# Performance work log

Measured on AMD Instinct MI355X. Metric: run time of the kernel, lower is better.

## Reference

```python
import jax, jax.numpy as jnp
import numpy as np

EPS = 1e-12  # F.normalize eps


def _normalize(x, axis):
    n = jnp.linalg.norm(x, axis=axis, keepdims=True)
    return x / jnp.maximum(n, EPS)


def _channel_equi_vec_normalize(x):
    # x: [B, C, 3, N]
    x_dir = _normalize(x, axis=2)
    x_norm = jnp.linalg.norm(x, axis=2, keepdims=True)   # [B,C,1,N]
    x_nn = _normalize(x_norm, axis=1)
    return x_dir * x_nn


def _se3_w(W):
    # append last column so each row sums to 1
    return jnp.concatenate([W, 1.0 - W.sum(-1, keepdims=True)], axis=-1)


def _vlin(W, x):
    # W: [O, C], x: [B, C, 3, N] -> [B, O, 3, N]
    return jnp.einsum('oc,bcvn->bovn', W, x)


def _slin(W, b, s):
    # W: [O, C], s: [B, C, N] -> [B, O, N]
    return jnp.einsum('oc,bcn->bon', W, s) + b[None, :, None]


def setup_inputs() -> dict:
    key = jax.random.key(0)
    ks = jax.random.split(key, 12)
    B, C, N = 16, 128, 4096
    scale = 0.05
    return {
        'v_input': jax.random.normal(ks[0], (B, C, 3, N), jnp.float32),
        's_input': jax.random.normal(ks[1], (B, C, N), jnp.float32),
        'weight': jax.random.normal(ks[2], (C, C - 1), jnp.float32) * scale,
        'sv_W': jax.random.normal(ks[3], (C, C), jnp.float32) * scale,
        'sv_b': jax.random.normal(ks[4], (C,), jnp.float32) * scale,
        'cross_weight': jax.random.normal(ks[5], (C, C - 1), jnp.float32) * scale,
        'crossfc_weight': jax.random.normal(ks[6], (C, 2 * C - 1), jnp.float32) * scale,
        'vsdir_weight': jax.random.normal(ks[7], (C, C), jnp.float32) * scale,
        'vs_W': jax.random.normal(ks[8], (C, C), jnp.float32) * scale,
        'vs_b': jax.random.normal(ks[9], (C,), jnp.float32) * scale,
        'ss_W': jax.random.normal(ks[10], (C, C), jnp.float32) * scale,
        'ss_b': jax.random.normal(ks[11], (C,), jnp.float32) * scale,
    }


def reference(v_input, s_input, weight, sv_W, sv_b, cross_weight, crossfc_weight,
              vsdir_weight, vs_W, vs_b, ss_W, ss_b):
    # --- vector output (se3 linear over channels) ---
    v_out = _vlin(_se3_w(weight), v_input)                       # [B,O,3,N]

    # --- scalar -> vector invariant scaling (se3: center, scale, re-add mean) ---
    s2v = _normalize(jnp.einsum('os,bsn->bon', sv_W, s_input) + sv_b[None, :, None], axis=1)
    v_mean = v_out.mean(axis=1, keepdims=True)
    v_out = (v_out - v_mean) * s2v[:, :, None, :] + v_mean

    # --- cross branch (se3) ---
    v_dual = _vlin(_se3_w(cross_weight), v_input)
    d_o = v_dual.mean(axis=1, keepdims=True)
    v_o = v_out.mean(axis=1, keepdims=True)
    v_cross = jnp.cross(_channel_equi_vec_normalize(v_dual - d_o), v_out - v_o, axis=2)
    v_cross = v_cross + v_out
    v_out = _vlin(_se3_w(crossfc_weight), jnp.concatenate([v_cross, v_out], axis=1))

    # --- scalar output ---
    v_sR = v_input - v_input.mean(axis=1, keepdims=True)         # se3 centering
    dual_dir = _normalize(jnp.einsum('oc,bcvn->bovn', vsdir_weight, v_sR), axis=2)
    s_from_v = _normalize((v_sR * dual_dir).sum(axis=2), axis=1)  # [B,C,N]
    s_from_v = _slin(vs_W, vs_b, s_from_v)
    s_from_s = _slin(ss_W, ss_b, s_input)
    s_output = s_from_s + s_from_v

    return (v_out, s_output)
```

## Files before the change

### kernel.cpp

```cpp
#include <hip/hip_runtime.h>
#include <math.h>

typedef __attribute__((ext_vector_type(8))) short short8;
typedef __attribute__((ext_vector_type(4))) float floatx4;

#define EPS 1e-12f

#define WS_AMAIN 0
#define WS_ASCAL 51200
#define WS_AFC   83968
#define WS_AVS   116736
#define WS_VDR_B 266240

__device__ __forceinline__ unsigned short f2bf(float f) {
  union { float f; unsigned u; } v; v.f = f;
  unsigned r = v.u + 0x7FFFu + ((v.u >> 16) & 1u);
  return (unsigned short)(r >> 16);
}
__device__ __forceinline__ float bf2f(unsigned u16) {
  union { unsigned u; float f; } v; v.u = u16 << 16;
  return v.f;
}

__device__ __forceinline__ float block_sum_256(float v, float* red) {
  const int t = threadIdx.x;
  red[t] = v;
  __syncthreads();
  for (int s = 128; s > 0; s >>= 1) {
    if (t < s) red[t] += red[t + s];
    __syncthreads();
  }
  float r = red[0];
  __syncthreads();
  return r;
}

__global__ __launch_bounds__(256) void k_pre(
    const float* __restrict__ weight, const float* __restrict__ sv_W,
    const float* __restrict__ cross_w, const float* __restrict__ crossfc_w,
    const float* __restrict__ vsdir_w, const float* __restrict__ vs_W,
    const float* __restrict__ ss_W, unsigned short* __restrict__ wsu,
    float* __restrict__ vdr) {
  __shared__ float red[256];
  const int o = blockIdx.x;
  const int t = threadIdx.x;

  float s1 = block_sum_256((t < 127) ? weight[o * 127 + t] : 0.f, red);
  if (t < 128)
    wsu[WS_AMAIN + o * 128 + t] = f2bf((t < 127) ? weight[o * 127 + t] : 1.f - s1);

  float s2 = block_sum_256((t < 127) ? cross_w[o * 127 + t] : 0.f, red);
  if (t < 128)
    wsu[WS_AMAIN + (128 + o) * 128 + t] = f2bf((t < 127) ? cross_w[o * 127 + t] : 1.f - s2);

  float s4 = block_sum_256((t < 128) ? vsdir_w[o * 128 + t] : 0.f, red);
  if (t < 128)
    wsu[WS_AMAIN + (256 + o) * 128 + t] = f2bf(vsdir_w[o * 128 + t]);
  if (t == 0) vdr[o] = s4;

  float s3 = block_sum_256((t < 255) ? crossfc_w[o * 255 + t] : 0.f, red);
  wsu[WS_AFC + o * 256 + t] = f2bf((t < 255) ? crossfc_w[o * 255 + t] : 1.f - s3);

  if (t < 128) {
    wsu[WS_ASCAL + o * 128 + t]         = f2bf(sv_W[o * 128 + t]);
    wsu[WS_ASCAL + (128 + o) * 128 + t] = f2bf(ss_W[o * 128 + t]);
    wsu[WS_AVS + o * 128 + t]           = f2bf(vs_W[o * 128 + t]);
  }
  if (o == 0) {
    if (t < 128) wsu[WS_AMAIN + 386 * 128 + t] = f2bf(1.f / 128.f);
    for (int l = t; l < 13 * 128; l += 256) wsu[WS_AMAIN + 387 * 128 + l] = 0;
  }
}

__global__ void k_mean(unsigned short* __restrict__ wsu) {
  const int g = blockIdx.x, c = threadIdx.x;
  float s = 0.f;
  for (int o = 0; o < 128; ++o) s += bf2f(wsu[WS_AMAIN + (g * 128 + o) * 128 + c]);
  wsu[WS_AMAIN + (384 + g) * 128 + c] = f2bf(s * (1.f / 128.f));
}

__global__ __launch_bounds__(512, 2) void k_main(
    const float* __restrict__ v_in, const float* __restrict__ s_in,
    const unsigned short* __restrict__ wsu, const float* __restrict__ vdr,
    const float* __restrict__ sv_b, const float* __restrict__ vs_b,
    const float* __restrict__ ss_b,
    float* __restrict__ v_out, float* __restrict__ s_out) {
  const int t = threadIdx.x;
  const int wave = t >> 6, lane = t & 63;
  const int q = lane >> 4, ln = lane & 15;
  const int cg = wave & 3;
  const int rg = wave >> 2;
  const int b = blockIdx.x >> 6;
  const int n0 = (blockIdx.x & 63) * 64;
  const int mycol = cg * 16 + ln;
  const int rb = rg * 64;
  const int rc = cg * 16 + ln;

  __shared__ __align__(16) unsigned short xB[192 * 136];
  __shared__ __align__(16) unsigned short v2B[192 * 136];
  __shared__ __align__(16) unsigned short sB[64 * 136];
  __shared__ float xred[6][2][64];

  {
    const float* vb = v_in + (size_t)b * (128 * 3 * 4096) + n0;
    for (int l = t; l < 6144; l += 512) {
      const int c = l / 48, r = l % 48;
      const int v = r >> 4, j4 = (r & 15) * 4;
      const float4 f = *(const float4*)(vb + (size_t)(c * 3 + v) * 4096 + j4);
      const int base = (v * 64 + j4) * 136 + c;
      xB[base]       = f2bf(f.x);
      xB[base + 136] = f2bf(f.y);
      xB[base + 272] = f2bf(f.z);
      xB[base + 408] = f2bf(f.w);
    }
    const float* sb = s_in + (size_t)b * (128 * 4096) + n0;
    for (int l = t; l < 2048; l += 512) {
      const int c = l >> 4, j4 = (l & 15) * 4;
      const float4 f = *(const float4*)(sb + (size_t)c * 4096 + j4);
      const int base = j4 * 136 + c;
      sB[base]       = f2bf(f.x);
      sB[base + 136] = f2bf(f.y);
      sB[base + 272] = f2bf(f.z);
      sB[base + 408] = f2bf(f.w);
    }
  }
  __syncthreads();

  floatx4 accS[8];
#pragma unroll
  for (int i = 0; i < 8; ++i) accS[i] = (floatx4){0.f, 0.f, 0.f, 0.f};
#pragma unroll
  for (int k = 0; k < 4; ++k) {
    const short8 bf = *(const short8*)(sB + mycol * 136 + k * 32 + q * 8);
    const unsigned short* ap = wsu + WS_ASCAL + (rb + ln) * 128 + k * 32 + q * 8;
#pragma unroll
    for (int mt = 0; mt < 4; ++mt)
      accS[mt] = __builtin_amdgcn_mfma_f32_16x16x32_bf16(
          *(const short8*)(ap + mt * 2048), bf, accS[mt], 0, 0, 0);
    const unsigned short* ap2 = ap + 128 * 128;
#pragma unroll
    for (int mt = 0; mt < 4; ++mt)
      accS[4 + mt] = __builtin_amdgcn_mfma_f32_16x16x32_bf16(
          *(const short8*)(ap2 + mt * 2048), bf, accS[4 + mt], 0, 0, 0);
  }
  float s2v[4][4], tssb[4][4];
  {
    float nrm = 0.f;
#pragma unroll
    for (int mt = 0; mt < 4; ++mt) {
      const float4 bb = *(const float4*)(sv_b + rb + mt * 16 + q * 4);
      const float* bp = (const float*)&bb;
#pragma unroll
      for (int r = 0; r < 4; ++r) {
        const float tv = accS[mt][r] + bp[r];
        s2v[mt][r] = tv;
        nrm += tv * tv;
      }
    }
    nrm += __shfl_xor(nrm, 16);
    nrm += __shfl_xor(nrm, 32);
    if (lane < 16) xred[0][rg][rc] = nrm;
    __syncthreads();
    const float ntot = xred[0][0][rc] + xred[0][1][rc];
    const float inv = 1.f / fmaxf(sqrtf(ntot), EPS);
#pragma unroll
    for (int mt = 0; mt < 4; ++mt)
#pragma unroll
      for (int r = 0; r < 4; ++r) s2v[mt][r] *= inv;
#pragma unroll
    for (int mt = 0; mt < 4; ++mt) {
      const float4 b1 = *(const float4*)(ss_b + rb + mt * 16 + q * 4);
      const float4 b2 = *(const float4*)(vs_b + rb + mt * 16 + q * 4);
      const float* p1 = (const float*)&b1;
      const float* p2 = (const float*)&b2;
#pragma unroll
      for (int r = 0; r < 4; ++r) tssb[mt][r] = accS[4 + mt][r] + p1[r] + p2[r];
    }
  }

  floatx4 accD[5][3];
#pragma unroll
  for (int i = 0; i < 5; ++i)
#pragma unroll
    for (int v = 0; v < 3; ++v) accD[i][v] = (floatx4){0.f, 0.f, 0.f, 0.f};
#pragma unroll
  for (int k = 0; k < 4; ++k) {
    short8 bfv[3];
#pragma unroll
    for (int v = 0; v < 3; ++v)
      bfv[v] = *(const short8*)(xB + (v * 64 + mycol) * 136 + k * 32 + q * 8);
    const unsigned short* ap = wsu + WS_AMAIN + (256 + rb + ln) * 128 + k * 32 + q * 8;
#pragma unroll
    for (int i = 0; i < 4; ++i) {
      const short8 a = *(const short8*)(ap + i * 2048);
#pragma unroll
      for (int v = 0; v < 3; ++v)
        accD[i][v] = __builtin_amdgcn_mfma_f32_16x16x32_bf16(a, bfv[v], accD[i][v], 0, 0, 0);
    }
    const unsigned short* am = wsu + WS_AMAIN + (384 + ln) * 128 + k * 32 + q * 8;
    const short8 a4 = *(const short8*)am;
#pragma unroll
    for (int v = 0; v < 3; ++v)
      accD[4][v] = __builtin_amdgcn_mfma_f32_16x16x32_bf16(a4, bfv[v], accD[4][v], 0, 0, 0);
  }
  float xm[3], vmn[3], dmn[3];
#pragma unroll
  for (int v = 0; v < 3; ++v) {
    vmn[v] = __shfl(accD[4][v][0], ln);
    dmn[v] = __shfl(accD[4][v][1], ln);
    xm[v]  = __shfl(accD[4][v][2], ln);
  }

  {
    float sfv[4][4];
    float ssum = 0.f;
#pragma unroll
    for (int mt = 0; mt < 4; ++mt) {
      const float4 rs4 = *(const float4*)(vdr + rb + mt * 16 + q * 4);
      const float* rp = (const float*)&rs4;
      uint2 pk[3];
#pragma unroll
      for (int v = 0; v < 3; ++v)
        pk[v] = *(const uint2*)(xB + (v * 64 + mycol) * 136 + rb + mt * 16 + q * 4);
#pragma unroll
      for (int r = 0; r < 4; ++r) {
        float d[3], xr[3];
#pragma unroll
        for (int v = 0; v < 3; ++v) {
          d[v] = accD[mt][v][r] - rp[r] * xm[v];
          const unsigned w = (r < 2) ? pk[v].x : pk[v].y;
          xr[v] = bf2f((w >> ((r & 1) * 16)) & 0xffffu) - xm[v];
        }
        const float n2 = d[0] * d[0] + d[1] * d[1] + d[2] * d[2];
        const float dinv = 1.f / fmaxf(sqrtf(n2), EPS);
        const float sv_ = (xr[0] * d[0] + xr[1] * d[1] + xr[2] * d[2]) * dinv;
        sfv[mt][r] = sv_;
        ssum += sv_ * sv_;
      }
    }
    ssum += __shfl_xor(ssum, 16);
    ssum += __shfl_xor(ssum, 32);
    if (lane < 16) xred[1][rg][rc] = ssum;
    __syncthreads();
    const float stot = xred[1][0][rc] + xred[1][1][rc];
    const float sinv = 1.f / fmaxf(sqrtf(stot), EPS);
#pragma unroll
    for (int mt = 0; mt < 4; ++mt) {
      const unsigned lo = (unsigned)f2bf(sfv[mt][0] * sinv) |
                          ((unsigned)f2bf(sfv[mt][1] * sinv) << 16);
      const unsigned hi = (unsigned)f2bf(sfv[mt][2] * sinv) |
                          ((unsigned)f2bf(sfv[mt][3] * sinv) << 16);
      *(uint2*)(sB + mycol * 136 + rb + mt * 16 + q * 4) = make_uint2(lo, hi);
    }
  }

  floatx4 accV[4][3];
#pragma unroll
  for (int i = 0; i < 4; ++i)
#pragma unroll
    for (int v = 0; v < 3; ++v) accV[i][v] = (floatx4){0.f, 0.f, 0.f, 0.f};
#pragma unroll
  for (int k = 0; k < 4; ++k) {
    short8 bfv[3];
#pragma unroll
    for (int v = 0; v < 3; ++v)
      bfv[v] = *(const short8*)(xB + (v * 64 + mycol) * 136 + k * 32 + q * 8);
    const unsigned short* ap = wsu + WS_AMAIN + (rb + ln) * 128 + k * 32 + q * 8;
#pragma unroll
    for (int mt = 0; mt < 4; ++mt) {
      const short8 a = *(const short8*)(ap + mt * 2048);
#pragma unroll
      for (int v = 0; v < 3; ++v)
        accV[mt][v] = __builtin_amdgcn_mfma_f32_16x16x32_bf16(a, bfv[v], accV[mt][v], 0, 0, 0);
    }
  }
  float v2m[3];
#pragma unroll
  for (int v = 0; v < 3; ++v) {
    float s = 0.f;
#pragma unroll
    for (int mt = 0; mt < 4; ++mt)
#pragma unroll
      for (int r = 0; r < 4; ++r) {
        const float val = (accV[mt][v][r] - vmn[v]) * s2v[mt][r] + vmn[v];
        accV[mt][v][r] = val;
        s += val;
      }
    s += __shfl_xor(s, 16);
    s += __shfl_xor(s, 32);
    if (lane < 16) xred[2 + v][rg][rc] = s;
  }
  __syncthreads();
#pragma unroll
  for (int v = 0; v < 3; ++v)
    v2m[v] = (xred[2 + v][0][rc] + xred[2 + v][1][rc]) * (1.f / 128.f);
#pragma unroll
  for (int mt = 0; mt < 4; ++mt)
#pragma unroll
    for (int v = 0; v < 3; ++v) {
      const unsigned lo = (unsigned)f2bf(accV[mt][v][0]) |
                          ((unsigned)f2bf(accV[mt][v][1]) << 16);
      const unsigned hi = (unsigned)f2bf(accV[mt][v][2]) |
                          ((unsigned)f2bf(accV[mt][v][3]) << 16);
      *(uint2*)(v2B + (v * 64 + mycol) * 136 + rb + mt * 16 + q * 4) = make_uint2(lo, hi);
    }

  floatx4 accW[4][3];
#pragma unroll
  for (int i = 0; i < 4; ++i)
#pragma unroll
    for (int v = 0; v < 3; ++v) accW[i][v] = (floatx4){0.f, 0.f, 0.f, 0.f};
#pragma unroll
  for (int k = 0; k < 4; ++k) {
    short8 bfv[3];
#pragma unroll
    for (int v = 0; v < 3; ++v)
      bfv[v] = *(const short8*)(xB + (v * 64 + mycol) * 136 + k * 32 + q * 8);
    const unsigned short* ap = wsu + WS_AMAIN + (128 + rb + ln) * 128 + k * 32 + q * 8;
#pragma unroll
    for (int mt = 0; mt < 4; ++mt) {
      const short8 a = *(const short8*)(ap + mt * 2048);
#pragma unroll
      for (int v = 0; v < 3; ++v)
        accW[mt][v] = __builtin_amdgcn_mfma_f32_16x16x32_bf16(a, bfv[v], accW[mt][v], 0, 0, 0);
    }
  }
  float an[4][4];
  float csum = 0.f;
#pragma unroll
  for (int mt = 0; mt < 4; ++mt)
#pragma unroll
    for (int r = 0; r < 4; ++r) {
      const float a0 = accW[mt][0][r] - dmn[0];
      const float a1 = accW[mt][1][r] - dmn[1];
      const float a2 = accW[mt][2][r] - dmn[2];
      accW[mt][0][r] = a0; accW[mt][1][r] = a1; accW[mt][2][r] = a2;
      const float n2 = a0 * a0 + a1 * a1 + a2 * a2;
      an[mt][r] = sqrtf(n2);
      csum += n2;
    }
  csum += __shfl_xor(csum, 16);
  csum += __shfl_xor(csum, 32);
  if (lane < 16) xred[5][rg][rc] = csum;
  __syncthreads();
  const float ctot = xred[5][0][rc] + xred[5][1][rc];
  const float cninv = 1.f / fmaxf(sqrtf(ctot), EPS);
#pragma unroll
  for (int mt = 0; mt < 4; ++mt) {
    float crv[3][4];
#pragma unroll
    for (int r = 0; r < 4; ++r) {
      const float sc = an[mt][r] / fmaxf(an[mt][r], EPS) * cninv;
      const float h0 = accW[mt][0][r] * sc;
      const float h1 = accW[mt][1][r] * sc;
      const float h2 = accW[mt][2][r] * sc;
      const float w0 = accV[mt][0][r], w1 = accV[mt][1][r], w2 = accV[mt][2][r];
      const float g0 = w0 - v2m[0], g1 = w1 - v2m[1], g2 = w2 - v2m[2];
      crv[0][r] = h1 * g2 - h2 * g1 + w0;
      crv[1][r] = h2 * g0 - h0 * g2 + w1;
      crv[2][r] = h0 * g1 - h1 * g0 + w2;
    }
#pragma unroll
    for (int v = 0; v < 3; ++v) {
      const unsigned lo = (unsigned)f2bf(crv[v][0]) | ((unsigned)f2bf(crv[v][1]) << 16);
      const unsigned hi = (unsigned)f2bf(crv[v][2]) | ((unsigned)f2bf(crv[v][3]) << 16);
      *(uint2*)(xB + (v * 64 + mycol) * 136 + rb + mt * 16 + q * 4) = make_uint2(lo, hi);
    }
  }
  __syncthreads();

  floatx4 accO[4][3];
  floatx4 accP[4];
#pragma unroll
  for (int i = 0; i < 4; ++i) {
    accP[i] = (floatx4){0.f, 0.f, 0.f, 0.f};
#pragma unroll
    for (int v = 0; v < 3; ++v) accO[i][v] = (floatx4){0.f, 0.f, 0.f, 0.f};
  }
#pragma unroll
  for (int ks = 0; ks < 8; ++ks) {
    const unsigned short* src = (ks < 4) ? xB : v2B;
    const int kk = ks & 3;
    short8 bfv[3];
#pragma unroll
    for (int v = 0; v < 3; ++v)
      bfv[v] = *(const short8*)(src + (v * 64 + mycol) * 136 + kk * 32 + q * 8);
    const unsigned short* afc = wsu + WS_AFC + (rb + ln) * 256 + ks * 32 + q * 8;
#pragma unroll
    for (int mt = 0; mt < 4; ++mt) {
      const short8 a = *(const short8*)(afc + mt * 4096);
#pragma unroll
      for (int v = 0; v < 3; ++v)
        accO[mt][v] = __builtin_amdgcn_mfma_f32_16x16x32_bf16(a, bfv[v], accO[mt][v], 0, 0, 0);
    }
    if (ks < 4) {
      const short8 bfs = *(const short8*)(sB + mycol * 136 + kk * 32 + q * 8);
      const unsigned short* avs = wsu + WS_AVS + (rb + ln) * 128 + kk * 32 + q * 8;
#pragma unroll
      for (int mt = 0; mt < 4; ++mt)
        accP[mt] = __builtin_amdgcn_mfma_f32_16x16x32_bf16(
            *(const short8*)(avs + mt * 2048), bfs, accP[mt], 0, 0, 0);
    }
  }

  const int gc = n0 + mycol;
  float* vob = v_out + (size_t)b * (128 * 3 * 4096) + gc;
  float* sob = s_out + (size_t)b * (128 * 4096) + gc;
#pragma unroll
  for (int mt = 0; mt < 4; ++mt)
#pragma unroll
    for (int r = 0; r < 4; ++r) {
      const int o = rb + mt * 16 + q * 4 + r;
#pragma unroll
      for (int v = 0; v < 3; ++v)
        vob[(size_t)(o * 3 + v) * 4096] = accO[mt][v][r];
      sob[(size_t)o * 4096] = accP[mt][r] + tssb[mt][r];
    }
}

extern "C" void kernel_launch(void* const* d_in, const int* in_sizes, int n_in,
                              void* d_out, int out_size, void* d_ws, size_t ws_size,
                              hipStream_t stream) {
  const float* v_in      = (const float*)d_in[0];
  const float* s_in      = (const float*)d_in[1];
  const float* weight    = (const float*)d_in[2];
  const float* sv_W      = (const float*)d_in[3];
  const float* sv_b      = (const float*)d_in[4];
  const float* cross_w   = (const float*)d_in[5];
  const float* crossfc_w = (const float*)d_in[6];
  const float* vsdir_w   = (const float*)d_in[7];
  const float* vs_W      = (const float*)d_in[8];
  const float* vs_b      = (const float*)d_in[9];
  const float* ss_W      = (const float*)d_in[10];
  const float* ss_b      = (const float*)d_in[11];

  float* out = (float*)d_out;
  float* v_out = out;
  float* s_out = out + (size_t)16 * 128 * 3 * 4096;
  unsigned short* wsu = (unsigned short*)d_ws;
  float* vdr = (float*)((char*)d_ws + WS_VDR_B);

  hipLaunchKernelGGL(k_pre, dim3(128), dim3(256), 0, stream,
                     weight, sv_W, cross_w, crossfc_w, vsdir_w, vs_W, ss_W, wsu, vdr);
  hipLaunchKernelGGL(k_mean, dim3(2), dim3(128), 0, stream, wsu);
  hipLaunchKernelGGL(k_main, dim3(1024), dim3(512), 0, stream,
                     v_in, s_in, wsu, vdr, sv_b, vs_b, ss_b, v_out, s_out);
}
```

Baseline: 410.1 us.

## Shrink k_main tile to 16 columns, compute channel means in-kernel, drop k_mean

Each block of k_main now handles 16 points instead of 64, and each of the 8 waves owns 16 output rows. This cuts register and shared-memory use so that up to 8 blocks can run per CU, and the grid grows to 4096 blocks with a swizzled block-to-tile mapping. The separate k_mean kernel is removed: the v_out and v_dual channel means are now computed algebraically from in-block reductions over 8 wave groups, and the mean rows of the weight matrix are zeroed. Packed bf16 conversion via v_cvt_pk_bf16_f32 replaces the scalar rounding. The trade-off is more cross-wave reductions and syncs, and the weight rows are reread per block across many more blocks.

```diff
diff --git a/kernel.cpp b/kernel.cpp
--- a/kernel.cpp
+++ b/kernel.cpp
@@ -20,6 +20,11 @@
 __device__ __forceinline__ float bf2f(unsigned u16) {
   union { unsigned u; float f; } v; v.u = u16 << 16;
   return v.f;
+}
+__device__ __forceinline__ unsigned pk2bf(float lo, float hi) {
+  unsigned r;
+  asm("v_cvt_pk_bf16_f32 %0, %1, %2" : "=v"(r) : "v"(lo), "v"(hi));
+  return r;
 }
 
 __device__ __forceinline__ float block_sum_256(float v, float* red) {
@@ -67,19 +72,12 @@
     wsu[WS_AVS + o * 128 + t]           = f2bf(vs_W[o * 128 + t]);
   }
   if (o == 0) {
+    for (int l = t; l < 16 * 128; l += 256) wsu[WS_AMAIN + 384 * 128 + l] = 0;
     if (t < 128) wsu[WS_AMAIN + 386 * 128 + t] = f2bf(1.f / 128.f);
-    for (int l = t; l < 13 * 128; l += 256) wsu[WS_AMAIN + 387 * 128 + l] = 0;
-  }
-}
-
-__global__ void k_mean(unsigned short* __restrict__ wsu) {
-  const int g = blockIdx.x, c = threadIdx.x;
-  float s = 0.f;
-  for (int o = 0; o < 128; ++o) s += bf2f(wsu[WS_AMAIN + (g * 128 + o) * 128 + c]);
-  wsu[WS_AMAIN + (384 + g) * 128 + c] = f2bf(s * (1.f / 128.f));
-}
-
-__global__ __launch_bounds__(512, 2) void k_main(
+  }
+}
+
+__global__ __launch_bounds__(512, 8) void k_main(
     const float* __restrict__ v_in, const float* __restrict__ s_in,
     const unsigned short* __restrict__ wsu, const float* __restrict__ vdr,
     const float* __restrict__ sv_b, const float* __restrict__ vs_b,
@@ -88,99 +86,90 @@
   const int t = threadIdx.x;
   const int wave = t >> 6, lane = t & 63;
   const int q = lane >> 4, ln = lane & 15;
-  const int cg = wave & 3;
-  const int rg = wave >> 2;
-  const int b = blockIdx.x >> 6;
-  const int n0 = (blockIdx.x & 63) * 64;
-  const int mycol = cg * 16 + ln;
-  const int rb = rg * 64;
-  const int rc = cg * 16 + ln;
-
-  __shared__ __align__(16) unsigned short xB[192 * 136];
-  __shared__ __align__(16) unsigned short v2B[192 * 136];
-  __shared__ __align__(16) unsigned short sB[64 * 136];
-  __shared__ float xred[6][2][64];
+  const int rg = wave;
+  const int rb = rg * 16;
+  const int bid = (int)(blockIdx.x & 7) * 512 + (int)(blockIdx.x >> 3);
+  const int b = bid >> 8;
+  const int n0 = (bid & 255) * 16;
+
+  __shared__ __align__(16) unsigned short xB[48 * 136];
+  __shared__ __align__(16) unsigned short v2B[48 * 136];
+  __shared__ __align__(16) unsigned short sB[16 * 136];
+  __shared__ float xred[12][8][16];
 
   {
     const float* vb = v_in + (size_t)b * (128 * 3 * 4096) + n0;
-    for (int l = t; l < 6144; l += 512) {
-      const int c = l / 48, r = l % 48;
-      const int v = r >> 4, j4 = (r & 15) * 4;
+    for (int l = t; l < 1536; l += 512) {
+      const int c = l / 12, rr = l % 12;
+      const int v = rr >> 2, j4 = (rr & 3) * 4;
       const float4 f = *(const float4*)(vb + (size_t)(c * 3 + v) * 4096 + j4);
-      const int base = (v * 64 + j4) * 136 + c;
-      xB[base]       = f2bf(f.x);
-      xB[base + 136] = f2bf(f.y);
-      xB[base + 272] = f2bf(f.z);
-      xB[base + 408] = f2bf(f.w);
+      const int base = (v * 16 + j4) * 136 + c;
+      const unsigned p01 = pk2bf(f.x, f.y);
+      const unsigned p23 = pk2bf(f.z, f.w);
+      xB[base]       = (unsigned short)p01;
+      xB[base + 136] = (unsigned short)(p01 >> 16);
+      xB[base + 272] = (unsigned short)p23;
+      xB[base + 408] = (unsigned short)(p23 >> 16);
     }
     const float* sb = s_in + (size_t)b * (128 * 4096) + n0;
-    for (int l = t; l < 2048; l += 512) {
-      const int c = l >> 4, j4 = (l & 15) * 4;
+    {
+      const int c = t >> 2, j4 = (t & 3) * 4;
       const float4 f = *(const float4*)(sb + (size_t)c * 4096 + j4);
       const int base = j4 * 136 + c;
-      sB[base]       = f2bf(f.x);
-      sB[base + 136] = f2bf(f.y);
-      sB[base + 272] = f2bf(f.z);
-      sB[base + 408] = f2bf(f.w);
-    }
-  }
-  __syncthreads();
-
-  floatx4 accS[8];
-#pragma unroll
-  for (int i = 0; i < 8; ++i) accS[i] = (floatx4){0.f, 0.f, 0.f, 0.f};
+      const unsigned p01 = pk2bf(f.x, f.y);
+      const unsigned p23 = pk2bf(f.z, f.w);
+      sB[base]       = (unsigned short)p01;
+      sB[base + 136] = (unsigned short)(p01 >> 16);
+      sB[base + 272] = (unsigned short)p23;
+      sB[base + 408] = (unsigned short)(p23 >> 16);
+    }
+  }
+  __syncthreads();
+
+  floatx4 accS[2];
+  accS[0] = (floatx4){0.f, 0.f, 0.f, 0.f};
+  accS[1] = (floatx4){0.f, 0.f, 0.f, 0.f};
 #pragma unroll
   for (int k = 0; k < 4; ++k) {
-    const short8 bf = *(const short8*)(sB + mycol * 136 + k * 32 + q * 8);
+    const short8 bf = *(const short8*)(sB + ln * 136 + k * 32 + q * 8);
     const unsigned short* ap = wsu + WS_ASCAL + (rb + ln) * 128 + k * 32 + q * 8;
-#pragma unroll
-    for (int mt = 0; mt < 4; ++mt)
-      accS[mt] = __builtin_amdgcn_mfma_f32_16x16x32_bf16(
-          *(const short8*)(ap + mt * 2048), bf, accS[mt], 0, 0, 0);
-    const unsigned short* ap2 = ap + 128 * 128;
-#pragma unroll
-    for (int mt = 0; mt < 4; ++mt)
-      accS[4 + mt] = __builtin_amdgcn_mfma_f32_16x16x32_bf16(
-          *(const short8*)(ap2 + mt * 2048), bf, accS[4 + mt], 0, 0, 0);
-  }
-  float s2v[4][4], tssb[4][4];
+    accS[0] = __builtin_amdgcn_mfma_f32_16x16x32_bf16(
+        *(const short8*)ap, bf, accS[0], 0, 0, 0);
+    accS[1] = __builtin_amdgcn_mfma_f32_16x16x32_bf16(
+        *(const short8*)(ap + 128 * 128), bf, accS[1], 0, 0, 0);
+  }
+  float s2v[4], tssb[4];
   {
     float nrm = 0.f;
-#pragma unroll
-    for (int mt = 0; mt < 4; ++mt) {
-      const float4 bb = *(const float4*)(sv_b + rb + mt * 16 + q * 4);
-      const float* bp = (const float*)&bb;
-#pragma unroll
-      for (int r = 0; r < 4; ++r) {
-        const float tv = accS[mt][r] + bp[r];
-        s2v[mt][r] = tv;
-        nrm += tv * tv;
-      }
+    const float4 bb = *(const float4*)(sv_b + rb + q * 4);
+    const float* bp = (const float*)&bb;
+#pragma unroll
+    for (int r = 0; r < 4; ++r) {
+      const float tv = accS[0][r] + bp[r];
+      s2v[r] = tv;
+      nrm += tv * tv;
     }
     nrm += __shfl_xor(nrm, 16);
     nrm += __shfl_xor(nrm, 32);
-    if (lane < 16) xred[0][rg][rc] = nrm;
+    if (lane < 16) xred[0][rg][ln] = nrm;
     __syncthreads();
-    const float ntot = xred[0][0][rc] + xred[0][1][rc];
+    float ntot = 0.f;
+#pragma unroll
+    for (int g = 0; g < 8; ++g) ntot += xred[0][g][ln];
     const float inv = 1.f / fmaxf(sqrtf(ntot), EPS);
 #pragma unroll
-    for (int mt = 0; mt < 4; ++mt)
-#pragma unroll
-      for (int r = 0; r < 4; ++r) s2v[mt][r] *= inv;
-#pragma unroll
-    for (int mt = 0; mt < 4; ++mt) {
-      const float4 b1 = *(const float4*)(ss_b + rb + mt * 16 + q * 4);
-      const float4 b2 = *(const float4*)(vs_b + rb + mt * 16 + q * 4);
-      const float* p1 = (const float*)&b1;
-      const float* p2 = (const float*)&b2;
-#pragma unroll
-      for (int r = 0; r < 4; ++r) tssb[mt][r] = accS[4 + mt][r] + p1[r] + p2[r];
-    }
-  }
-
-  floatx4 accD[5][3];
-#pragma unroll
-  for (int i = 0; i < 5; ++i)
+    for (int r = 0; r < 4; ++r) s2v[r] *= inv;
+    const float4 b1 = *(const float4*)(ss_b + rb + q * 4);
+    const float4 b2 = *(const float4*)(vs_b + rb + q * 4);
+    const float* p1 = (const float*)&b1;
+    const float* p2 = (const float*)&b2;
+#pragma unroll
+    for (int r = 0; r < 4; ++r) tssb[r] = accS[1][r] + p1[r] + p2[r];
+  }
+
+  floatx4 accD[2][3];
+#pragma unroll
+  for (int i = 0; i < 2; ++i)
 #pragma unroll
     for (int v = 0; v < 3; ++v) accD[i][v] = (floatx4){0.f, 0.f, 0.f, 0.f};
 #pragma unroll
@@ -188,173 +177,176 @@
     short8 bfv[3];
 #pragma unroll
     for (int v = 0; v < 3; ++v)
-      bfv[v] = *(const short8*)(xB + (v * 64 + mycol) * 136 + k * 32 + q * 8);
+      bfv[v] = *(const short8*)(xB + (v * 16 + ln) * 136 + k * 32 + q * 8);
     const unsigned short* ap = wsu + WS_AMAIN + (256 + rb + ln) * 128 + k * 32 + q * 8;
-#pragma unroll
-    for (int i = 0; i < 4; ++i) {
-      const short8 a = *(const short8*)(ap + i * 2048);
-#pragma unroll
-      for (int v = 0; v < 3; ++v)
-        accD[i][v] = __builtin_amdgcn_mfma_f32_16x16x32_bf16(a, bfv[v], accD[i][v], 0, 0, 0);
-    }
+    const short8 a0 = *(const short8*)ap;
     const unsigned short* am = wsu + WS_AMAIN + (384 + ln) * 128 + k * 32 + q * 8;
-    const short8 a4 = *(const short8*)am;
-#pragma unroll
-    for (int v = 0; v < 3; ++v)
-      accD[4][v] = __builtin_amdgcn_mfma_f32_16x16x32_bf16(a4, bfv[v], accD[4][v], 0, 0, 0);
-  }
-  float xm[3], vmn[3], dmn[3];
-#pragma unroll
-  for (int v = 0; v < 3; ++v) {
-    vmn[v] = __shfl(accD[4][v][0], ln);
-    dmn[v] = __shfl(accD[4][v][1], ln);
-    xm[v]  = __shfl(accD[4][v][2], ln);
-  }
-
-  {
-    float sfv[4][4];
+    const short8 a1 = *(const short8*)am;
+#pragma unroll
+    for (int v = 0; v < 3; ++v) {
+      accD[0][v] = __builtin_amdgcn_mfma_f32_16x16x32_bf16(a0, bfv[v], accD[0][v], 0, 0, 0);
+      accD[1][v] = __builtin_amdgcn_mfma_f32_16x16x32_bf16(a1, bfv[v], accD[1][v], 0, 0, 0);
+    }
+  }
+  float xm[3];
+#pragma unroll
+  for (int v = 0; v < 3; ++v) xm[v] = __shfl(accD[1][v][2], ln);
+
+  {
+    float sfv[4];
     float ssum = 0.f;
-#pragma unroll
-    for (int mt = 0; mt < 4; ++mt) {
-      const float4 rs4 = *(const float4*)(vdr + rb + mt * 16 + q * 4);
-      const float* rp = (const float*)&rs4;
-      uint2 pk[3];
-#pragma unroll
-      for (int v = 0; v < 3; ++v)
-        pk[v] = *(const uint2*)(xB + (v * 64 + mycol) * 136 + rb + mt * 16 + q * 4);
-#pragma unroll
-      for (int r = 0; r < 4; ++r) {
-        float d[3], xr[3];
-#pragma unroll
-        for (int v = 0; v < 3; ++v) {
-          d[v] = accD[mt][v][r] - rp[r] * xm[v];
-          const unsigned w = (r < 2) ? pk[v].x : pk[v].y;
-          xr[v] = bf2f((w >> ((r & 1) * 16)) & 0xffffu) - xm[v];
-        }
-        const float n2 = d[0] * d[0] + d[1] * d[1] + d[2] * d[2];
-        const float dinv = 1.f / fmaxf(sqrtf(n2), EPS);
-        const float sv_ = (xr[0] * d[0] + xr[1] * d[1] + xr[2] * d[2]) * dinv;
-        sfv[mt][r] = sv_;
-        ssum += sv_ * sv_;
+    const float4 rs4 = *(const float4*)(vdr + rb + q * 4);
+    const float* rp = (const float*)&rs4;
+    uint2 pk[3];
+#pragma unroll
+    for (int v = 0; v < 3; ++v)
+      pk[v] = *(const uint2*)(xB + (v * 16 + ln) * 136 + rb + q * 4);
+#pragma unroll
+    for (int r = 0; r < 4; ++r) {
+      float d[3], xr[3];
+#pragma unroll
+      for (int v = 0; v < 3; ++v) {
+        d[v] = accD[0][v][r] - rp[r] * xm[v];
+        const unsigned w = (r < 2) ? pk[v].x : pk[v].y;
+        xr[v] = bf2f((w >> ((r & 1) * 16)) & 0xffffu) - xm[v];
       }
+      const float n2 = d[0] * d[0] + d[1] * d[1] + d[2] * d[2];
+      const float dinv = 1.f / fmaxf(sqrtf(n2), EPS);
+      const float sv_ = (xr[0] * d[0] + xr[1] * d[1] + xr[2] * d[2]) * dinv;
+      sfv[r] = sv_;
+      ssum += sv_ * sv_;
     }
     ssum += __shfl_xor(ssum, 16);
     ssum += __shfl_xor(ssum, 32);
-    if (lane < 16) xred[1][rg][rc] = ssum;
+    if (lane < 16) xred[1][rg][ln] = ssum;
     __syncthreads();
-    const float stot = xred[1][0][rc] + xred[1][1][rc];
+    float stot = 0.f;
+#pragma unroll
+    for (int g = 0; g < 8; ++g) stot += xred[1][g][ln];
     const float sinv = 1.f / fmaxf(sqrtf(stot), EPS);
-#pragma unroll
-    for (int mt = 0; mt < 4; ++mt) {
-      const unsigned lo = (unsigned)f2bf(sfv[mt][0] * sinv) |
-                          ((unsigned)f2bf(sfv[mt][1] * sinv) << 16);
-      const unsigned hi = (unsigned)f2bf(sfv[mt][2] * sinv) |
-                          ((unsigned)f2bf(sfv[mt][3] * sinv) << 16);
-      *(uint2*)(sB + mycol * 136 + rb + mt * 16 + q * 4) = make_uint2(lo, hi);
-    }
-  }
-
-  floatx4 accV[4][3];
-#pragma unroll
-  for (int i = 0; i < 4; ++i)
-#pragma unroll
-    for (int v = 0; v < 3; ++v) accV[i][v] = (floatx4){0.f, 0.f, 0.f, 0.f};
+    const unsigned lo = pk2bf(sfv[0] * sinv, sfv[1] * sinv);
+    const unsigned hi = pk2bf(sfv[2] * sinv, sfv[3] * sinv);
+    *(uint2*)(sB + ln * 136 + rb + q * 4) = make_uint2(lo, hi);
+  }
+
+  floatx4 accV[3];
+#pragma unroll
+  for (int v = 0; v < 3; ++v) accV[v] = (floatx4){0.f, 0.f, 0.f, 0.f};
 #pragma unroll
   for (int k = 0; k < 4; ++k) {
     short8 bfv[3];
 #pragma unroll
     for (int v = 0; v < 3; ++v)
-      bfv[v] = *(const short8*)(xB + (v * 64 + mycol) * 136 + k * 32 + q * 8);
+      bfv[v] = *(const short8*)(xB + (v * 16 + ln) * 136 + k * 32 + q * 8);
     const unsigned short* ap = wsu + WS_AMAIN + (rb + ln) * 128 + k * 32 + q * 8;
-#pragma unroll
-    for (int mt = 0; mt < 4; ++mt) {
-      const short8 a = *(const short8*)(ap + mt * 2048);
-#pragma unroll
-      for (int v = 0; v < 3; ++v)
-        accV[mt][v] = __builtin_amdgcn_mfma_f32_16x16x32_bf16(a, bfv[v], accV[mt][v], 0, 0, 0);
-    }
-  }
-  float v2m[3];
+    const short8 a = *(const short8*)ap;
+#pragma unroll
+    for (int v = 0; v < 3; ++v)
+      accV[v] = __builtin_amdgcn_mfma_f32_16x16x32_bf16(a, bfv[v], accV[v], 0, 0, 0);
+  }
 #pragma unroll
   for (int v = 0; v < 3; ++v) {
-    float s = 0.f;
-#pragma unroll
-    for (int mt = 0; mt < 4; ++mt)
-#pragma unroll
-      for (int r = 0; r < 4; ++r) {
-        const float val = (accV[mt][v][r] - vmn[v]) * s2v[mt][r] + vmn[v];
-        accV[mt][v][r] = val;
-        s += val;
-      }
-    s += __shfl_xor(s, 16);
-    s += __shfl_xor(s, 32);
-    if (lane < 16) xred[2 + v][rg][rc] = s;
-  }
-  __syncthreads();
-#pragma unroll
-  for (int v = 0; v < 3; ++v)
-    v2m[v] = (xred[2 + v][0][rc] + xred[2 + v][1][rc]) * (1.f / 128.f);
-#pragma unroll
-  for (int mt = 0; mt < 4; ++mt)
+    float sa = 0.f, sb2 = 0.f;
+#pragma unroll
+    for (int r = 0; r < 4; ++r) {
+      sa += accV[v][r];
+      sb2 += s2v[r] * accV[v][r];
+    }
+    sa += __shfl_xor(sa, 16);   sa += __shfl_xor(sa, 32);
+    sb2 += __shfl_xor(sb2, 16); sb2 += __shfl_xor(sb2, 32);
+    if (lane < 16) { xred[2 + v][rg][ln] = sa; xred[5 + v][rg][ln] = sb2; }
+  }
+  {
+    float sc = s2v[0] + s2v[1] + s2v[2] + s2v[3];
+    sc += __shfl_xor(sc, 16);
+    sc += __shfl_xor(sc, 32);
+    if (lane < 16) xred[8][rg][ln] = sc;
+  }
+  __syncthreads();
+  float vmn[3], v2m[3];
+  {
+    float sct = 0.f;
+#pragma unroll
+    for (int g = 0; g < 8; ++g) sct += xred[8][g][ln];
 #pragma unroll
     for (int v = 0; v < 3; ++v) {
-      const unsigned lo = (unsigned)f2bf(accV[mt][v][0]) |
-                          ((unsigned)f2bf(accV[mt][v][1]) << 16);
-      const unsigned hi = (unsigned)f2bf(accV[mt][v][2]) |
-                          ((unsigned)f2bf(accV[mt][v][3]) << 16);
-      *(uint2*)(v2B + (v * 64 + mycol) * 136 + rb + mt * 16 + q * 4) = make_uint2(lo, hi);
-    }
-
-  floatx4 accW[4][3];
-#pragma unroll
-  for (int i = 0; i < 4; ++i)
-#pragma unroll
-    for (int v = 0; v < 3; ++v) accW[i][v] = (floatx4){0.f, 0.f, 0.f, 0.f};
+      float sat = 0.f, sbt = 0.f;
+#pragma unroll
+      for (int g = 0; g < 8; ++g) { sat += xred[2 + v][g][ln]; sbt += xred[5 + v][g][ln]; }
+      vmn[v] = sat * (1.f / 128.f);
+      v2m[v] = (sbt + vmn[v] * (128.f - sct)) * (1.f / 128.f);
+    }
+  }
+#pragma unroll
+  for (int v = 0; v < 3; ++v) {
+#pragma unroll
+    for (int r = 0; r < 4; ++r)
+      accV[v][r] = (accV[v][r] - vmn[v]) * s2v[r] + vmn[v];
+    const unsigned lo = pk2bf(accV[v][0], accV[v][1]);
+    const unsigned hi = pk2bf(accV[v][2], accV[v][3]);
+    *(uint2*)(v2B + (v * 16 + ln) * 136 + rb + q * 4) = make_uint2(lo, hi);
+  }
+
+  floatx4 accW[3];
+#pragma unroll
+  for (int v = 0; v < 3; ++v) accW[v] = (floatx4){0.f, 0.f, 0.f, 0.f};
 #pragma unroll
   for (int k = 0; k < 4; ++k) {
     short8 bfv[3];
 #pragma unroll
     for (int v = 0; v < 3; ++v)
-      bfv[v] = *(const short8*)(xB + (v * 64 + mycol) * 136 + k * 32 + q * 8);
+      bfv[v] = *(const short8*)(xB + (v * 16 + ln) * 136 + k * 32 + q * 8);
     const unsigned short* ap = wsu + WS_AMAIN + (128 + rb + ln) * 128 + k * 32 + q * 8;
-#pragma unroll
-    for (int mt = 0; mt < 4; ++mt) {
-      const short8 a = *(const short8*)(ap + mt * 2048);
-#pragma unroll
-      for (int v = 0; v < 3; ++v)
-        accW[mt][v] = __builtin_amdgcn_mfma_f32_16x16x32_bf16(a, bfv[v], accW[mt][v], 0, 0, 0);
-    }
-  }
-  float an[4][4];
-  float csum = 0.f;
-#pragma unroll
-  for (int mt = 0; mt < 4; ++mt)
+    const short8 a = *(const short8*)ap;
+#pragma unroll
+    for (int v = 0; v < 3; ++v)
+      accW[v] = __builtin_amdgcn_mfma_f32_16x16x32_bf16(a, bfv[v], accW[v], 0, 0, 0);
+  }
+  {
+    float ssq = 0.f;
+#pragma unroll
+    for (int v = 0; v < 3; ++v) {
+      float s = 0.f;
+#pragma unroll
+      for (int r = 0; r < 4; ++r) {
+        s += accW[v][r];
+        ssq += accW[v][r] * accW[v][r];
+      }
+      s += __shfl_xor(s, 16);
+      s += __shfl_xor(s, 32);
+      if (lane < 16) xred[9 + v][rg][ln] = s;
+    }
+    ssq += __shfl_xor(ssq, 16);
+    ssq += __shfl_xor(ssq, 32);
+    if (lane < 16) xred[0][rg][ln] = ssq;
+  }
+  __syncthreads();
+  float dmn[3];
+  {
+#pragma unroll
+    for (int v = 0; v < 3; ++v) {
+      float s = 0.f;
+#pragma unroll
+      for (int g = 0; g < 8; ++g) s += xred[9 + v][g][ln];
+      dmn[v] = s * (1.f / 128.f);
+    }
+  }
+  {
+    float sqt = 0.f;
+#pragma unroll
+    for (int g = 0; g < 8; ++g) sqt += xred[0][g][ln];
+    const float ctot = sqt - 128.f * (dmn[0] * dmn[0] + dmn[1] * dmn[1] + dmn[2] * dmn[2]);
+    const float cninv = 1.f / fmaxf(sqrtf(ctot), EPS);
+    float crv[3][4];
 #pragma unroll
     for (int r = 0; r < 4; ++r) {
-      const float a0 = accW[mt][0][r] - dmn[0];
-      const float a1 = accW[mt][1][r] - dmn[1];
-      const float a2 = accW[mt][2][r] - dmn[2];
-      accW[mt][0][r] = a0; accW[mt][1][r] = a1; accW[mt][2][r] = a2;
-      const float n2 = a0 * a0 + a1 * a1 + a2 * a2;
-      an[mt][r] = sqrtf(n2);
-      csum += n2;
-    }
-  csum += __shfl_xor(csum, 16);
-  csum += __shfl_xor(csum, 32);
-  if (lane < 16) xred[5][rg][rc] = csum;
-  __syncthreads();
-  const float ctot = xred[5][0][rc] + xred[5][1][rc];
-  const float cninv = 1.f / fmaxf(sqrtf(ctot), EPS);
-#pragma unroll
-  for (int mt = 0; mt < 4; ++mt) {
-    float crv[3][4];
-#pragma unroll
-    for (int r = 0; r < 4; ++r) {
-      const float sc = an[mt][r] / fmaxf(an[mt][r], EPS) * cninv;
-      const float h0 = accW[mt][0][r] * sc;
-      const float h1 = accW[mt][1][r] * sc;
-      const float h2 = accW[mt][2][r] * sc;
-      const float w0 = accV[mt][0][r], w1 = accV[mt][1][r], w2 = accV[mt][2][r];
+      const float a0 = accW[0][r] - dmn[0];
+      const float a1 = accW[1][r] - dmn[1];
+      const float a2 = accW[2][r] - dmn[2];
+      const float an = sqrtf(a0 * a0 + a1 * a1 + a2 * a2);
+      const float sc = an / fmaxf(an, EPS) * cninv;
+      const float h0 = a0 * sc, h1 = a1 * sc, h2 = a2 * sc;
+      const float w0 = accV[0][r], w1 = accV[1][r], w2 = accV[2][r];
       const float g0 = w0 - v2m[0], g1 = w1 - v2m[1], g2 = w2 - v2m[2];
       crv[0][r] = h1 * g2 - h2 * g1 + w0;
       crv[1][r] = h2 * g0 - h0 * g2 + w1;
@@ -362,21 +354,17 @@
     }
 #pragma unroll
     for (int v = 0; v < 3; ++v) {
-      const unsigned lo = (unsigned)f2bf(crv[v][0]) | ((unsigned)f2bf(crv[v][1]) << 16);
-      const unsigned hi = (unsigned)f2bf(crv[v][2]) | ((unsigned)f2bf(crv[v][3]) << 16);
-      *(uint2*)(xB + (v * 64 + mycol) * 136 + rb + mt * 16 + q * 4) = make_uint2(lo, hi);
-    }
-  }
-  __syncthreads();
-
-  floatx4 accO[4][3];
-  floatx4 accP[4];
-#pragma unroll
-  for (int i = 0; i < 4; ++i) {
-    accP[i] = (floatx4){0.f, 0.f, 0.f, 0.f};
-#pragma unroll
-    for (int v = 0; v < 3; ++v) accO[i][v] = (floatx4){0.f, 0.f, 0.f, 0.f};
-  }
+      const unsigned lo = pk2bf(crv[v][0], crv[v][1]);
+      const unsigned hi = pk2bf(crv[v][2], crv[v][3]);
+      *(uint2*)(xB + (v * 16 + ln) * 136 + rb + q * 4) = make_uint2(lo, hi);
+    }
+  }
+  __syncthreads();
+
+  floatx4 accO[3];
+  floatx4 accP = (floatx4){0.f, 0.f, 0.f, 0.f};
+#pragma unroll
+  for (int v = 0; v < 3; ++v) accO[v] = (floatx4){0.f, 0.f, 0.f, 0.f};
 #pragma unroll
   for (int ks = 0; ks < 8; ++ks) {
     const unsigned short* src = (ks < 4) ? xB : v2B;
@@ -384,38 +372,31 @@
     short8 bfv[3];
 #pragma unroll
     for (int v = 0; v < 3; ++v)
-      bfv[v] = *(const short8*)(src + (v * 64 + mycol) * 136 + kk * 32 + q * 8);
+      bfv[v] = *(const short8*)(src + (v * 16 + ln) * 136 + kk * 32 + q * 8);
     const unsigned short* afc = wsu + WS_AFC + (rb + ln) * 256 + ks * 32 + q * 8;
-#pragma unroll
-    for (int mt = 0; mt < 4; ++mt) {
-      const short8 a = *(const short8*)(afc + mt * 4096);
-#pragma unroll
-      for (int v = 0; v < 3; ++v)
-        accO[mt][v] = __builtin_amdgcn_mfma_f32_16x16x32_bf16(a, bfv[v], accO[mt][v], 0, 0, 0);
-    }
+    const short8 a = *(const short8*)afc;
+#pragma unroll
+    for (int v = 0; v < 3; ++v)
+      accO[v] = __builtin_amdgcn_mfma_f32_16x16x32_bf16(a, bfv[v], accO[v], 0, 0, 0);
     if (ks < 4) {
-      const short8 bfs = *(const short8*)(sB + mycol * 136 + kk * 32 + q * 8);
+      const short8 bfs = *(const short8*)(sB + ln * 136 + kk * 32 + q * 8);
       const unsigned short* avs = wsu + WS_AVS + (rb + ln) * 128 + kk * 32 + q * 8;
-#pragma unroll
-      for (int mt = 0; mt < 4; ++mt)
-        accP[mt] = __builtin_amdgcn_mfma_f32_16x16x32_bf16(
-            *(const short8*)(avs + mt * 2048), bfs, accP[mt], 0, 0, 0);
-    }
-  }
-
-  const int gc = n0 + mycol;
+      accP = __builtin_amdgcn_mfma_f32_16x16x32_bf16(
+          *(const short8*)(avs), bfs, accP, 0, 0, 0);
+    }
+  }
+
+  const int gc = n0 + ln;
   float* vob = v_out + (size_t)b * (128 * 3 * 4096) + gc;
   float* sob = s_out + (size_t)b * (128 * 4096) + gc;
 #pragma unroll
-  for (int mt = 0; mt < 4; ++mt)
-#pragma unroll
-    for (int r = 0; r < 4; ++r) {
-      const int o = rb + mt * 16 + q * 4 + r;
-#pragma unroll
-      for (int v = 0; v < 3; ++v)
-        vob[(size_t)(o * 3 + v) * 4096] = accO[mt][v][r];
-      sob[(size_t)o * 4096] = accP[mt][r] + tssb[mt][r];
-    }
+  for (int r = 0; r < 4; ++r) {
+    const int o = rb + q * 4 + r;
+#pragma unroll
+    for (int v = 0; v < 3; ++v)
+      vob[(size_t)(o * 3 + v) * 4096] = accO[v][r];
+    sob[(size_t)o * 4096] = accP[r] + tssb[r];
+  }
 }
 
 extern "C" void kernel_launch(void* const* d_in, const int* in_sizes, int n_in,
@@ -442,7 +423,6 @@
 
   hipLaunchKernelGGL(k_pre, dim3(128), dim3(256), 0, stream,
                      weight, sv_W, cross_w, crossfc_w, vsdir_w, vs_W, ss_W, wsu, vdr);
-  hipLaunchKernelGGL(k_mean, dim3(2), dim3(128), 0, stream, wsu);
-  hipLaunchKernelGGL(k_main, dim3(1024), dim3(512), 0, stream,
+  hipLaunchKernelGGL(k_main, dim3(4096), dim3(512), 0, stream,
                      v_in, s_in, wsu, vdr, sv_b, vs_b, ss_b, v_out, s_out);
 }
```

New measurement: 453.8 us. +10.7%, slower.
